# Kernel tuning notes

Measured on AMD Instinct MI355X. Metric: run time of the kernel, lower is better.

## Reference

```python
import jax, jax.numpy as jnp
import numpy as np

BATCH = 1_000_000
NUM_BINS = 37  # num_classes == 37 -> ranges [0, 13, 26, 37]
STARTS = jnp.array([0, 13, 26], dtype=jnp.int32)
ENDS = jnp.array([13, 26, 37], dtype=jnp.int32)
NEG_INF = jnp.float32(-1e30)
LOG_CLAMP = -100.0  # torch BCE clamps log terms at -100


def setup_inputs() -> dict:
    key = jax.random.key(0)
    k1, k2, k3 = jax.random.split(key, 3)
    preds = jax.random.normal(k1, (BATCH, NUM_BINS), dtype=jnp.float32)
    labels = jax.random.normal(k2, (BATCH, NUM_BINS), dtype=jnp.float32)
    obj_classes = jax.random.randint(k3, (BATCH,), 0, 3, dtype=jnp.int32)
    weights = jnp.ones((3,), dtype=jnp.float32)
    return {"preds": preds, "labels": labels, "weights": weights,
            "obj_classes": obj_classes}


def reference(preds, labels, weights, obj_classes):
    # Per-sample ragged slice [start, end) expressed as a mask over the 37 bins.
    idx = jnp.arange(NUM_BINS)
    s = STARTS[obj_classes][:, None]  # (B, 1)
    e = ENDS[obj_classes][:, None]    # (B, 1)
    mask = (idx >= s) & (idx < e)     # (B, 37)

    # Softmax restricted to the active slice (masked positions -> -inf logits).
    logp = jax.nn.log_softmax(jnp.where(mask, preds, NEG_INF), axis=-1)
    p = jnp.exp(logp)
    t = jax.nn.softmax(jnp.where(mask, labels, NEG_INF), axis=-1)

    # BCE(p, t) summed over the slice (size_average=False):
    # -(t*log p + (1-t)*log(1-p)), with torch-style log clamping at -100.
    logp_c = jnp.maximum(logp, LOG_CLAMP)
    log1mp = jnp.maximum(jnp.log1p(-p), LOG_CLAMP)
    bce = jnp.where(mask, -(t * logp_c + (1.0 - t) * log1mp), 0.0)

    per_sample = bce.sum(axis=-1) * weights[obj_classes]  # (B,)
    losses = jax.ops.segment_sum(per_sample, obj_classes, num_segments=3)
    total = losses.sum() / jnp.float32(preds.shape[0])
    return (total[None], losses[0][None], losses[1][None], losses[2][None])
```

## Files before the change

kernel.cpp:

```cpp
#include <hip/hip_runtime.h>

constexpr int BATCH  = 1000000;
constexpr int NBINS  = 37;
constexpr int TPB    = 128;
constexpr int ROWS   = 128;
constexpr int TFLOAT = ROWS * NBINS;
constexpr int TVEC   = TFLOAT / 4;
constexpr int KFULL  = TVEC / TPB;
constexpr int VREM   = TVEC - KFULL*TPB;
constexpr int NTILES = (BATCH + ROWS - 1) / ROWS;
constexpr int NBLK   = 512;
constexpr int QT     = NTILES / NBLK;
constexpr int RT     = NTILES % NBLK;
constexpr float NEG_BIG  = -1e30f;
constexpr float LOGCLAMP = -100.0f;

__global__ __launch_bounds__(TPB, 1)
void adviser_loss_kernel(const float* __restrict__ preds,
                         const float* __restrict__ labels,
                         const float* __restrict__ weights,
                         const int* __restrict__ obj,
                         float* __restrict__ out)
{
    __shared__ float buf[2][2][TFLOAT];
    __shared__ float cls_sum[3];

    const int tid = threadIdx.x;
    const int b   = blockIdx.x;
    if (tid < 3) cls_sum[tid] = 0.0f;

    const int cnt = QT + (b < RT ? 1 : 0);
    const int t0  = b * QT + min(b, RT);

    const float w0 = weights[0], w1 = weights[1], w2 = weights[2];

    auto stage = [&](int sel, int t) {
        const int rowbase = t * ROWS;
        const int nrows   = min(ROWS, BATCH - rowbase);
        const float4* gp = (const float4*)(preds  + (size_t)rowbase * NBINS);
        const float4* gl = (const float4*)(labels + (size_t)rowbase * NBINS);
        if (nrows == ROWS) {
            #pragma unroll
            for (int k = 0; k < KFULL; ++k) {
                const int i = tid + k * TPB;
                __builtin_amdgcn_global_load_lds(
                    (const __attribute__((address_space(1))) void*)(gp + i),
                    (__attribute__((address_space(3))) void*)(&buf[sel][0][i * 4]),
                    16, 0, 0);
                __builtin_amdgcn_global_load_lds(
                    (const __attribute__((address_space(1))) void*)(gl + i),
                    (__attribute__((address_space(3))) void*)(&buf[sel][1][i * 4]),
                    16, 0, 0);
            }
            if (tid < VREM) {
                const int i = KFULL * TPB + tid;
                ((float4*)buf[sel][0])[i] = gp[i];
                ((float4*)buf[sel][1])[i] = gl[i];
            }
        } else {
            const int nv = (nrows * NBINS) >> 2;
            for (int i = tid; i < nv; i += TPB) {
                ((float4*)buf[sel][0])[i] = gp[i];
                ((float4*)buf[sel][1])[i] = gl[i];
            }
        }
    };

    stage(0, t0);
    int ccur = obj[min(t0 * ROWS + tid, BATCH - 1)];
    __syncthreads();

    float a0 = 0.0f, a1 = 0.0f, a2 = 0.0f;
    int cur = 0;

    for (int ti = 0; ti < cnt; ++ti) {
        const int t       = t0 + ti;
        const int rowbase = t * ROWS;
        const int nrows   = min(ROWS, BATCH - rowbase);

        int cnext = ccur;
        if (ti + 1 < cnt) {
            stage(cur ^ 1, t + 1);
            cnext = obj[min((t + 1) * ROWS + tid, BATCH - 1)];
        }

        const bool valid = (tid < nrows);
        const int   c = ccur;
        const float w = (c == 0) ? w0 : ((c == 1) ? w1 : w2);
        const int   s = 13 * c;
        const int   L = (c == 2) ? 11 : 13;
        const int   base = tid * NBINS + s;

        const float* P = buf[cur][0];
        const float* T = buf[cur][1];

        float pv[13], ep[13], et[13];
        float Z = 0.0f, Zt = 0.0f;
        #pragma unroll
        for (int j = 0; j < 13; ++j) {
            const float x = (j < L) ? P[base + j] : NEG_BIG;
            const float y = (j < L) ? T[base + j] : NEG_BIG;
            pv[j] = x;
            ep[j] = __expf(x);  Z  += ep[j];
            et[j] = __expf(y);  Zt += et[j];
        }
        const float logZ  = __logf(Z);
        const float rcpZ  = __builtin_amdgcn_rcpf(Z);
        const float rcpZt = __builtin_amdgcn_rcpf(Zt);

        float acc = 0.0f;
        #pragma unroll
        for (int j = 0; j < 13; ++j) {
            const float logp = pv[j] - logZ;
            const float p    = ep[j] * rcpZ;
            const float ca   = fmaxf(logp, LOGCLAMP);
            const float cb   = fmaxf(__logf(fmaxf(1.0f - p, 0.0f)), LOGCLAMP);
            const float t_   = et[j] * rcpZt;
            acc += cb + t_ * (ca - cb);
        }
        const float per = valid ? (-acc) * w : 0.0f;
        a0 += (c == 0) ? per : 0.0f;
        a1 += (c == 1) ? per : 0.0f;
        a2 += (c == 2) ? per : 0.0f;

        __syncthreads();
        cur ^= 1;
        ccur = cnext;
    }

    #pragma unroll
    for (int off = 32; off > 0; off >>= 1) {
        a0 += __shfl_down(a0, off, 64);
        a1 += __shfl_down(a1, off, 64);
        a2 += __shfl_down(a2, off, 64);
    }
    if ((tid & 63) == 0) {
        atomicAdd(&cls_sum[0], a0);
        atomicAdd(&cls_sum[1], a1);
        atomicAdd(&cls_sum[2], a2);
    }
    __syncthreads();
    if (tid == 0) {
        const float s0 = cls_sum[0], s1 = cls_sum[1], s2 = cls_sum[2];
        atomicAdd(&out[1], s0);
        atomicAdd(&out[2], s1);
        atomicAdd(&out[3], s2);
        atomicAdd(&out[0], (s0 + s1 + s2) * (1.0f / (float)BATCH));
    }
}

extern "C" void kernel_launch(void* const* d_in, const int* in_sizes, int n_in,
                              void* d_out, int out_size, void* d_ws, size_t ws_size,
                              hipStream_t stream) {
    const float* preds   = (const float*)d_in[0];
    const float* labels  = (const float*)d_in[1];
    const float* weights = (const float*)d_in[2];
    const int*   obj     = (const int*)d_in[3];
    float* out = (float*)d_out;

    hipMemsetAsync(out, 0, (size_t)out_size * sizeof(float), stream);
    adviser_loss_kernel<<<NBLK, TPB, 0, stream>>>(preds, labels, weights, obj, out);
}
```

Before: 331.7 us.

## Use single-wave blocks with vmcnt-based double buffering instead of barriers

Each block becomes a single 64-thread wavefront handling 64-row tiles across 1024 blocks. Barrier-based double buffering is replaced by explicit s_waitcnt vmcnt counting on direct global-to-LDS loads, and class ids are now also staged through LDS. This removes __syncthreads and the shared-memory reduction and keeps the next tile's loads in flight during compute. It relies on BATCH being a multiple of 64 with no tail handling, and on a hand-counted vmcnt value (21) being correct for the issued loads.

```diff
diff --git a/kernel.cpp b/kernel.cpp
--- a/kernel.cpp
+++ b/kernel.cpp
@@ -2,18 +2,20 @@
 
 constexpr int BATCH  = 1000000;
 constexpr int NBINS  = 37;
-constexpr int TPB    = 128;
-constexpr int ROWS   = 128;
+constexpr int TPB    = 64;
+constexpr int ROWS   = 64;
 constexpr int TFLOAT = ROWS * NBINS;
-constexpr int TVEC   = TFLOAT / 4;
-constexpr int KFULL  = TVEC / TPB;
-constexpr int VREM   = TVEC - KFULL*TPB;
-constexpr int NTILES = (BATCH + ROWS - 1) / ROWS;
-constexpr int NBLK   = 512;
+constexpr int TV16   = 9;
+constexpr int REMOFF = TV16 * TPB * 4;
+constexpr int NTILES = BATCH / ROWS;
+constexpr int NBLK   = 1024;
 constexpr int QT     = NTILES / NBLK;
 constexpr int RT     = NTILES % NBLK;
 constexpr float NEG_BIG  = -1e30f;
 constexpr float LOGCLAMP = -100.0f;
+
+#define AS1 __attribute__((address_space(1)))
+#define AS3 __attribute__((address_space(3)))
 
 __global__ __launch_bounds__(TPB, 1)
 void adviser_loss_kernel(const float* __restrict__ preds,
@@ -22,77 +24,48 @@
                          const int* __restrict__ obj,
                          float* __restrict__ out)
 {
-    __shared__ float buf[2][2][TFLOAT];
-    __shared__ float cls_sum[3];
+    __shared__ float bufP[2][TFLOAT];
+    __shared__ float bufL[2][TFLOAT];
+    __shared__ int   clsb[2][ROWS];
 
     const int tid = threadIdx.x;
     const int b   = blockIdx.x;
-    if (tid < 3) cls_sum[tid] = 0.0f;
-
     const int cnt = QT + (b < RT ? 1 : 0);
     const int t0  = b * QT + min(b, RT);
 
     const float w0 = weights[0], w1 = weights[1], w2 = weights[2];
 
     auto stage = [&](int sel, int t) {
-        const int rowbase = t * ROWS;
-        const int nrows   = min(ROWS, BATCH - rowbase);
-        const float4* gp = (const float4*)(preds  + (size_t)rowbase * NBINS);
-        const float4* gl = (const float4*)(labels + (size_t)rowbase * NBINS);
-        if (nrows == ROWS) {
-            #pragma unroll
-            for (int k = 0; k < KFULL; ++k) {
-                const int i = tid + k * TPB;
-                __builtin_amdgcn_global_load_lds(
-                    (const __attribute__((address_space(1))) void*)(gp + i),
-                    (__attribute__((address_space(3))) void*)(&buf[sel][0][i * 4]),
-                    16, 0, 0);
-                __builtin_amdgcn_global_load_lds(
-                    (const __attribute__((address_space(1))) void*)(gl + i),
-                    (__attribute__((address_space(3))) void*)(&buf[sel][1][i * 4]),
-                    16, 0, 0);
-            }
-            if (tid < VREM) {
-                const int i = KFULL * TPB + tid;
-                ((float4*)buf[sel][0])[i] = gp[i];
-                ((float4*)buf[sel][1])[i] = gl[i];
-            }
-        } else {
-            const int nv = (nrows * NBINS) >> 2;
-            for (int i = tid; i < nv; i += TPB) {
-                ((float4*)buf[sel][0])[i] = gp[i];
-                ((float4*)buf[sel][1])[i] = gl[i];
-            }
+        const size_t rb = (size_t)t * ROWS;
+        const float* gp = preds  + rb * NBINS;
+        const float* gl = labels + rb * NBINS;
+        #pragma unroll
+        for (int k = 0; k < TV16; ++k) {
+            const int i = (tid + k * TPB) * 4;
+            __builtin_amdgcn_global_load_lds((const AS1 void*)(gp + i),
+                                             (AS3 void*)(&bufP[sel][i]), 16, 0, 0);
+            __builtin_amdgcn_global_load_lds((const AS1 void*)(gl + i),
+                                             (AS3 void*)(&bufL[sel][i]), 16, 0, 0);
         }
+        const int r = REMOFF + tid;
+        __builtin_amdgcn_global_load_lds((const AS1 void*)(gp + r),
+                                         (AS3 void*)(&bufP[sel][r]), 4, 0, 0);
+        __builtin_amdgcn_global_load_lds((const AS1 void*)(gl + r),
+                                         (AS3 void*)(&bufL[sel][r]), 4, 0, 0);
+        __builtin_amdgcn_global_load_lds((const AS1 void*)(obj + rb + tid),
+                                         (AS3 void*)(&clsb[sel][tid]), 4, 0, 0);
     };
 
-    stage(0, t0);
-    int ccur = obj[min(t0 * ROWS + tid, BATCH - 1)];
-    __syncthreads();
+    float a0 = 0.0f, a1 = 0.0f, a2 = 0.0f;
 
-    float a0 = 0.0f, a1 = 0.0f, a2 = 0.0f;
-    int cur = 0;
-
-    for (int ti = 0; ti < cnt; ++ti) {
-        const int t       = t0 + ti;
-        const int rowbase = t * ROWS;
-        const int nrows   = min(ROWS, BATCH - rowbase);
-
-        int cnext = ccur;
-        if (ti + 1 < cnt) {
-            stage(cur ^ 1, t + 1);
-            cnext = obj[min((t + 1) * ROWS + tid, BATCH - 1)];
-        }
-
-        const bool valid = (tid < nrows);
-        const int   c = ccur;
+    auto compute = [&](int sel) {
+        const int   c = clsb[sel][tid];
         const float w = (c == 0) ? w0 : ((c == 1) ? w1 : w2);
         const int   s = 13 * c;
         const int   L = (c == 2) ? 11 : 13;
         const int   base = tid * NBINS + s;
-
-        const float* P = buf[cur][0];
-        const float* T = buf[cur][1];
+        const float* P = bufP[sel];
+        const float* T = bufL[sel];
 
         float pv[13], ep[13], et[13];
         float Z = 0.0f, Zt = 0.0f;
@@ -118,15 +91,23 @@
             const float t_   = et[j] * rcpZt;
             acc += cb + t_ * (ca - cb);
         }
-        const float per = valid ? (-acc) * w : 0.0f;
+        const float per = (-acc) * w;
         a0 += (c == 0) ? per : 0.0f;
         a1 += (c == 1) ? per : 0.0f;
         a2 += (c == 2) ? per : 0.0f;
+    };
 
-        __syncthreads();
-        cur ^= 1;
-        ccur = cnext;
+    stage(0, t0);
+
+    for (int ti = 0; ti < cnt - 1; ++ti) {
+        stage((ti + 1) & 1, t0 + ti + 1);
+        asm volatile("s_waitcnt vmcnt(21)" ::: "memory");
+        __builtin_amdgcn_sched_barrier(0);
+        compute(ti & 1);
     }
+    asm volatile("s_waitcnt vmcnt(0)" ::: "memory");
+    __builtin_amdgcn_sched_barrier(0);
+    compute((cnt - 1) & 1);
 
     #pragma unroll
     for (int off = 32; off > 0; off >>= 1) {
@@ -134,18 +115,11 @@
         a1 += __shfl_down(a1, off, 64);
         a2 += __shfl_down(a2, off, 64);
     }
-    if ((tid & 63) == 0) {
-        atomicAdd(&cls_sum[0], a0);
-        atomicAdd(&cls_sum[1], a1);
-        atomicAdd(&cls_sum[2], a2);
-    }
-    __syncthreads();
     if (tid == 0) {
-        const float s0 = cls_sum[0], s1 = cls_sum[1], s2 = cls_sum[2];
-        atomicAdd(&out[1], s0);
-        atomicAdd(&out[2], s1);
-        atomicAdd(&out[3], s2);
-        atomicAdd(&out[0], (s0 + s1 + s2) * (1.0f / (float)BATCH));
+        atomicAdd(&out[1], a0);
+        atomicAdd(&out[2], a1);
+        atomicAdd(&out[3], a2);
+        atomicAdd(&out[0], (a0 + a1 + a2) * (1.0f / (float)BATCH));
     }
 }
 
```

After: 358.9 us. 1.08x slower.

## Switch to per-wave tiles with register prefetch and no block barriers

Applied to the files above, without the earlier changes.

Each wavefront now owns its own 64-row tile slice in LDS and prefetches the next tile into registers (float4 loads plus a tail element) while computing the current one. This replaces the block-wide double-buffered global_load_lds staging and the per-tile __syncthreads. Blocks grow to 256 threads with two blocks per CU for more occupancy. The cost is much higher register pressure (18 float4 prefetch registers), an extra register-to-LDS store pass, and reliance on BATCH dividing evenly by 64. Without a wave barrier, write-after-read ordering in LDS between iterations rests on in-order wave execution.

```diff
diff --git a/kernel.cpp b/kernel.cpp
--- a/kernel.cpp
+++ b/kernel.cpp
@@ -2,104 +2,86 @@
 
 constexpr int BATCH  = 1000000;
 constexpr int NBINS  = 37;
-constexpr int TPB    = 128;
-constexpr int ROWS   = 128;
-constexpr int TFLOAT = ROWS * NBINS;
-constexpr int TVEC   = TFLOAT / 4;
-constexpr int KFULL  = TVEC / TPB;
-constexpr int VREM   = TVEC - KFULL*TPB;
-constexpr int NTILES = (BATCH + ROWS - 1) / ROWS;
+constexpr int TPB    = 256;
+constexpr int WPB    = 4;
+constexpr int ROWS   = 64;
+constexpr int TDW    = ROWS * NBINS;
+constexpr int NV     = 9;
+constexpr int REMDW  = NV * 64 * 4;
 constexpr int NBLK   = 512;
-constexpr int QT     = NTILES / NBLK;
-constexpr int RT     = NTILES % NBLK;
+constexpr int NWAVES = NBLK * WPB;
+constexpr int NTILES = BATCH / ROWS;
 constexpr float NEG_BIG  = -1e30f;
 constexpr float LOGCLAMP = -100.0f;
 
-__global__ __launch_bounds__(TPB, 1)
+__global__ __launch_bounds__(TPB, 2)
 void adviser_loss_kernel(const float* __restrict__ preds,
                          const float* __restrict__ labels,
                          const float* __restrict__ weights,
                          const int* __restrict__ obj,
                          float* __restrict__ out)
 {
-    __shared__ float buf[2][2][TFLOAT];
+    __shared__ float lds[WPB][2][TDW];
     __shared__ float cls_sum[3];
 
-    const int tid = threadIdx.x;
-    const int b   = blockIdx.x;
+    const int tid  = threadIdx.x;
+    const int lane = tid & 63;
+    const int w    = tid >> 6;
+    const int gw   = blockIdx.x * WPB + w;
+
     if (tid < 3) cls_sum[tid] = 0.0f;
-
-    const int cnt = QT + (b < RT ? 1 : 0);
-    const int t0  = b * QT + min(b, RT);
+    __syncthreads();
 
     const float w0 = weights[0], w1 = weights[1], w2 = weights[2];
 
-    auto stage = [&](int sel, int t) {
-        const int rowbase = t * ROWS;
-        const int nrows   = min(ROWS, BATCH - rowbase);
-        const float4* gp = (const float4*)(preds  + (size_t)rowbase * NBINS);
-        const float4* gl = (const float4*)(labels + (size_t)rowbase * NBINS);
-        if (nrows == ROWS) {
-            #pragma unroll
-            for (int k = 0; k < KFULL; ++k) {
-                const int i = tid + k * TPB;
-                __builtin_amdgcn_global_load_lds(
-                    (const __attribute__((address_space(1))) void*)(gp + i),
-                    (__attribute__((address_space(3))) void*)(&buf[sel][0][i * 4]),
-                    16, 0, 0);
-                __builtin_amdgcn_global_load_lds(
-                    (const __attribute__((address_space(1))) void*)(gl + i),
-                    (__attribute__((address_space(3))) void*)(&buf[sel][1][i * 4]),
-                    16, 0, 0);
-            }
-            if (tid < VREM) {
-                const int i = KFULL * TPB + tid;
-                ((float4*)buf[sel][0])[i] = gp[i];
-                ((float4*)buf[sel][1])[i] = gl[i];
-            }
-        } else {
-            const int nv = (nrows * NBINS) >> 2;
-            for (int i = tid; i < nv; i += TPB) {
-                ((float4*)buf[sel][0])[i] = gp[i];
-                ((float4*)buf[sel][1])[i] = gl[i];
-            }
+    float* myP = &lds[w][0][0];
+    float* myT = &lds[w][1][0];
+
+    float4 Pv[NV], Lv[NV];
+    float  Pf = 0.0f, Lf = 0.0f;
+    int    creg = 0;
+
+    auto prefetch = [&](int t) {
+        const float4* gp = (const float4*)(preds  + (size_t)t * TDW);
+        const float4* gl = (const float4*)(labels + (size_t)t * TDW);
+        #pragma unroll
+        for (int k = 0; k < NV; ++k) {
+            Pv[k] = gp[lane + k * 64];
+            Lv[k] = gl[lane + k * 64];
         }
+        Pf = ((const float*)gp)[REMDW + lane];
+        Lf = ((const float*)gl)[REMDW + lane];
+        creg = obj[t * ROWS + lane];
     };
 
-    stage(0, t0);
-    int ccur = obj[min(t0 * ROWS + tid, BATCH - 1)];
-    __syncthreads();
+    float a0 = 0.0f, a1 = 0.0f, a2 = 0.0f;
 
-    float a0 = 0.0f, a1 = 0.0f, a2 = 0.0f;
-    int cur = 0;
+    prefetch(gw);
+    for (int t = gw; t < NTILES; t += NWAVES) {
+        #pragma unroll
+        for (int k = 0; k < NV; ++k) {
+            ((float4*)myP)[lane + k * 64] = Pv[k];
+            ((float4*)myT)[lane + k * 64] = Lv[k];
+        }
+        myP[REMDW + lane] = Pf;
+        myT[REMDW + lane] = Lf;
+        const int c = creg;
 
-    for (int ti = 0; ti < cnt; ++ti) {
-        const int t       = t0 + ti;
-        const int rowbase = t * ROWS;
-        const int nrows   = min(ROWS, BATCH - rowbase);
+        const int nt = t + NWAVES;
+        if (nt < NTILES) prefetch(nt);
+        __builtin_amdgcn_sched_barrier(0);
 
-        int cnext = ccur;
-        if (ti + 1 < cnt) {
-            stage(cur ^ 1, t + 1);
-            cnext = obj[min((t + 1) * ROWS + tid, BATCH - 1)];
-        }
-
-        const bool valid = (tid < nrows);
-        const int   c = ccur;
-        const float w = (c == 0) ? w0 : ((c == 1) ? w1 : w2);
-        const int   s = 13 * c;
-        const int   L = (c == 2) ? 11 : 13;
-        const int   base = tid * NBINS + s;
-
-        const float* P = buf[cur][0];
-        const float* T = buf[cur][1];
+        const float wt = (c == 0) ? w0 : ((c == 1) ? w1 : w2);
+        const int   s  = 13 * c;
+        const int   L  = (c == 2) ? 11 : 13;
+        const int   base = lane * NBINS + s;
 
         float pv[13], ep[13], et[13];
         float Z = 0.0f, Zt = 0.0f;
         #pragma unroll
         for (int j = 0; j < 13; ++j) {
-            const float x = (j < L) ? P[base + j] : NEG_BIG;
-            const float y = (j < L) ? T[base + j] : NEG_BIG;
+            const float x = (j < L) ? myP[base + j] : NEG_BIG;
+            const float y = (j < L) ? myT[base + j] : NEG_BIG;
             pv[j] = x;
             ep[j] = __expf(x);  Z  += ep[j];
             et[j] = __expf(y);  Zt += et[j];
@@ -118,14 +100,10 @@
             const float t_   = et[j] * rcpZt;
             acc += cb + t_ * (ca - cb);
         }
-        const float per = valid ? (-acc) * w : 0.0f;
+        const float per = (-acc) * wt;
         a0 += (c == 0) ? per : 0.0f;
         a1 += (c == 1) ? per : 0.0f;
         a2 += (c == 2) ? per : 0.0f;
-
-        __syncthreads();
-        cur ^= 1;
-        ccur = cnext;
     }
 
     #pragma unroll
@@ -134,7 +112,7 @@
         a1 += __shfl_down(a1, off, 64);
         a2 += __shfl_down(a2, off, 64);
     }
-    if ((tid & 63) == 0) {
+    if (lane == 0) {
         atomicAdd(&cls_sum[0], a0);
         atomicAdd(&cls_sum[1], a1);
         atomicAdd(&cls_sum[2], a2);
```

New measurement: 349.4 us. 1.05x slower.
